# Kernel tuning notes

Hardware: AMD Instinct MI355X
Metric: run time of the kernel (lower is better)

The kernel has to match this reference:

```python
import jax, jax.numpy as jnp
import numpy as np

N_NODES = 100000
N_EDGES = 1600000
HID = 128
EDGE_DIM = 32
GN_EPS = 1e-5


def setup_inputs() -> dict:
    key = jax.random.key(0)
    ks = jax.random.split(key, 8)
    s = 0.05
    return {
        "x": jax.random.normal(ks[0], (N_NODES, HID), jnp.float32),
        "edge_index": jax.random.randint(ks[1], (2, N_EDGES), 0, N_NODES, jnp.int64),
        "edge_attr": jax.random.normal(ks[2], (N_EDGES, EDGE_DIM), jnp.float32),
        "edge_lin_W": jax.random.normal(ks[3], (EDGE_DIM, HID), jnp.float32) * s,
        "edge_lin_b": jnp.zeros((HID,), jnp.float32),
        "mlp_W1": jax.random.normal(ks[4], (HID, HID), jnp.float32) * s,
        "mlp_b1": jnp.zeros((HID,), jnp.float32),
        "mlp_W2": jax.random.normal(ks[5], (HID, HID), jnp.float32) * s,
        "mlp_b2": jnp.zeros((HID,), jnp.float32),
        "gn_weight": jnp.ones((HID,), jnp.float32),
        "gn_bias": jnp.zeros((HID,), jnp.float32),
        "gn_mean_scale": jnp.ones((HID,), jnp.float32),
    }


def reference(x, edge_index, edge_attr, edge_lin_W, edge_lin_b,
              mlp_W1, mlp_b1, mlp_W2, mlp_b2,
              gn_weight, gn_bias, gn_mean_scale):
    src, dst = edge_index[0], edge_index[1]
    # GINEConv message: ReLU(x_j + Lin(edge_attr)), sum-aggregated at dst
    e = edge_attr @ edge_lin_W + edge_lin_b            # [E, HID]
    msg = jax.nn.relu(x[src] + e)                      # [E, HID]
    agg = jax.ops.segment_sum(msg, dst, num_segments=x.shape[0])  # [N, HID]
    # update MLP on (1+eps)*x + agg, eps = 0
    h = agg + x
    h = jax.nn.relu(h @ mlp_W1 + mlp_b1) @ mlp_W2 + mlp_b2
    # GraphNorm with batch=None -> single graph: global node stats
    mean = jnp.mean(h, axis=0, keepdims=True)          # [1, HID]
    sub = h - gn_mean_scale * mean
    var = jnp.mean(sub * sub, axis=0, keepdims=True)
    out = gn_weight * sub / jnp.sqrt(var + GN_EPS) + gn_bias
    # final ReLU; dropout is identity at eval
    return jax.nn.relu(out)
```

## Files before the change

### kernel.cpp

```cpp
#include <hip/hip_runtime.h>
#include <stdint.h>

#define HID 128
#define EDIM 32

typedef __attribute__((ext_vector_type(8))) short bf16x8;
typedef __attribute__((ext_vector_type(4))) float f4_t;

static __device__ __forceinline__ unsigned short f2bf(float f) {
  union { float f; unsigned int u; } v; v.f = f;
  return (unsigned short)((v.u + 0x7fffu + ((v.u >> 16) & 1u)) >> 16);
}

static __device__ __forceinline__ float bf2f(short s) {
  union { unsigned int u; float f; } v;
  v.u = ((unsigned int)(unsigned short)s) << 16;
  return v.f;
}

static __device__ __forceinline__ void atomAddF(float* p, float v) {
#if defined(__gfx950__) || defined(__gfx942__) || defined(__gfx90a__)
  unsafeAtomicAdd(p, v);
#else
  atomicAdd(p, v);
#endif
}

__global__ __launch_bounds__(256) void hist_xperm(const int* __restrict__ ei,
                                                  const float* __restrict__ x,
                                                  unsigned int* __restrict__ counts,
                                                  unsigned short* __restrict__ xPerm,
                                                  int nE, int nNodes, int doPerm) {
  int tid = blockIdx.x * blockDim.x + threadIdx.x;
  const int stride = gridDim.x * blockDim.x;
  for (int i = tid; i < nE; i += stride) atomicAdd(&counts[ei[nE + i]], 1u);
  if (doPerm) {
    const int nCh = nNodes * 16;
    for (int j = tid; j < nCh; j += stride) {
      const int node = j >> 4, g = j & 15;
      const float* xp = x + (size_t)node * HID + g;
      bf16x8 o;
#pragma unroll
      for (int k = 0; k < 8; ++k) o[k] = (short)f2bf(xp[k * 16]);
      *(bf16x8*)(xPerm + (size_t)node * HID + g * 8) = o;
    }
  }
}

__global__ __launch_bounds__(1024) void chunk_sum(const unsigned int* __restrict__ counts,
                                                  unsigned int* __restrict__ chunkSum, int N) {
  __shared__ unsigned int wsum[16];
  const int tid = threadIdx.x;
  const int i = blockIdx.x * 1024 + tid;
  unsigned int v = (i < N) ? counts[i] : 0u;
#pragma unroll
  for (int d = 1; d < 64; d <<= 1) v += (unsigned int)__shfl_xor((int)v, d);
  if ((tid & 63) == 0) wsum[tid >> 6] = v;
  __syncthreads();
  if (tid < 16) {
    unsigned int t = wsum[tid];
#pragma unroll
    for (int d = 1; d < 16; d <<= 1) t += (unsigned int)__shfl_xor((int)t, d);
    if (tid == 0) chunkSum[blockIdx.x] = t;
  }
}

__global__ __launch_bounds__(256) void scan_chunks(const unsigned int* __restrict__ chunkSum,
                                                   unsigned int* __restrict__ chunkOff,
                                                   unsigned int* __restrict__ offsets,
                                                   int nChunks, int N) {
  __shared__ unsigned int wsum[4];
  const int tid = threadIdx.x, lane = tid & 63, w = tid >> 6;
  unsigned int v = (tid < nChunks) ? chunkSum[tid] : 0u;
  unsigned int s = v;
#pragma unroll
  for (int d = 1; d < 64; d <<= 1) {
    unsigned int t = (unsigned int)__shfl_up((int)s, d);
    if (lane >= d) s += t;
  }
  if (lane == 63) wsum[w] = s;
  __syncthreads();
  unsigned int wOff = 0;
  for (int k = 0; k < w; ++k) wOff += wsum[k];
  if (tid < nChunks) chunkOff[tid] = wOff + s - v;
  if (tid == nChunks - 1) offsets[N] = wOff + s;
}

__global__ __launch_bounds__(1024) void scan_local(const unsigned int* __restrict__ counts,
                                                   const unsigned int* __restrict__ chunkOff,
                                                   unsigned int* __restrict__ offsets,
                                                   unsigned int* __restrict__ cursors, int N) {
  __shared__ unsigned int wsum[16];
  const int tid = threadIdx.x, lane = tid & 63, w = tid >> 6;
  const int i = blockIdx.x * 1024 + tid;
  unsigned int v = (i < N) ? counts[i] : 0u;
  unsigned int s = v;
#pragma unroll
  for (int d = 1; d < 64; d <<= 1) {
    unsigned int t = (unsigned int)__shfl_up((int)s, d);
    if (lane >= d) s += t;
  }
  if (lane == 63) wsum[w] = s;
  __syncthreads();
  unsigned int wOff = 0;
  for (int k = 0; k < w; ++k) wOff += wsum[k];
  if (i < N) {
    const unsigned int ex = chunkOff[blockIdx.x] + wOff + (s - v);
    offsets[i] = ex;
    cursors[i] = ex;
  }
}

__global__ __launch_bounds__(256) void scatter_conv(const int* __restrict__ ei,
                                                    const float* __restrict__ ea,
                                                    unsigned int* __restrict__ cursors,
                                                    unsigned int* __restrict__ sortedSrc,
                                                    unsigned short* __restrict__ eaSorted,
                                                    int nE) {
  const int lane = threadIdx.x & 63;
  const int q = lane & 3;
  int t = blockIdx.x * blockDim.x + threadIdx.x;
  const int eStride = (gridDim.x * blockDim.x) >> 2;
  for (int e = t >> 2; e < nE; e += eStride) {
    unsigned int pos = 0;
    if (q == 0) {
      const int d = ei[nE + e];
      pos = atomicAdd(&cursors[d], 1u);
      sortedSrc[pos] = (unsigned int)ei[e];
    }
    pos = (unsigned int)__shfl((int)pos, lane & ~3);
    const f4_t* ap = (const f4_t*)(ea + (size_t)e * EDIM + q * 8);
    f4_t a0 = __builtin_nontemporal_load(ap);
    f4_t a1 = __builtin_nontemporal_load(ap + 1);
    bf16x8 o;
#pragma unroll
    for (int k = 0; k < 4; ++k) { o[k] = (short)f2bf(a0[k]); o[k + 4] = (short)f2bf(a1[k]); }
    *(bf16x8*)(eaSorted + (size_t)pos * EDIM + q * 8) = o;
  }
}

__global__ __launch_bounds__(256) void scatter_min(const int* __restrict__ ei,
                                                   unsigned int* __restrict__ cursors,
                                                   unsigned int* __restrict__ sortedEid,
                                                   unsigned int* __restrict__ sortedSrc,
                                                   int nE) {
  int i = blockIdx.x * blockDim.x + threadIdx.x;
  const int stride = gridDim.x * blockDim.x;
  for (; i < nE; i += stride) {
    const int d = ei[nE + i];
    const unsigned int pos = atomicAdd(&cursors[d], 1u);
    sortedEid[pos] = (unsigned int)i;
    sortedSrc[pos] = (unsigned int)ei[i];
  }
}

template <int MODE>
__global__ __launch_bounds__(256) void agg_kernel(
    const float* __restrict__ x, const unsigned short* __restrict__ xPerm,
    const float* __restrict__ ea, const unsigned short* __restrict__ eaSorted,
    const float* __restrict__ W, const float* __restrict__ bias,
    const unsigned int* __restrict__ offsets, const unsigned int* __restrict__ sortedEid,
    const unsigned int* __restrict__ sortedSrc, float* __restrict__ h,
    int nNodes) {
  const int lane = threadIdx.x & 63;
  const int l15 = lane & 15;
  const int lq  = lane >> 4;

  bf16x8 Wf[8];
  float bv[8];
#pragma unroll
  for (int nt = 0; nt < 8; ++nt) {
#pragma unroll
    for (int j = 0; j < 8; ++j)
      Wf[nt][j] = (short)f2bf(W[(8 * lq + j) * HID + 16 * nt + l15]);
    bv[nt] = bias[16 * nt + l15];
  }

  const int wavesPerBlk = blockDim.x >> 6;
  int waveId = blockIdx.x * wavesPerBlk + ((int)threadIdx.x >> 6);
  const int nWaves = gridDim.x * wavesPerBlk;

  for (int n = waveId; n < nNodes; n += nWaves) {
    const unsigned int beg = offsets[n];
    const unsigned int end = offsets[n + 1];

    float accv[8] = {0, 0, 0, 0, 0, 0, 0, 0};

    for (unsigned int base = beg; base < end; base += 16) {
      bf16x8 af = {0, 0, 0, 0, 0, 0, 0, 0};
      const unsigned int slotA = base + (unsigned int)l15;
      if (slotA < end) {
        if (MODE == 2) {
          const unsigned int eidA = __builtin_nontemporal_load(&sortedEid[slotA]);
          const float* ap = ea + (size_t)eidA * EDIM + 8 * lq;
          f4_t a0 = *(const f4_t*)ap;
          f4_t a1 = *(const f4_t*)(ap + 4);
#pragma unroll
          for (int j = 0; j < 4; ++j) { af[j] = (short)f2bf(a0[j]); af[j + 4] = (short)f2bf(a1[j]); }
        } else {
          af = __builtin_nontemporal_load(
              (const bf16x8*)(eaSorted + (size_t)slotA * EDIM + lq * 8));
        }
      }

      unsigned int s_r[4];
      bf16x8 xg[4];
#pragma unroll
      for (int r = 0; r < 4; ++r) {
        unsigned int slot = base + (unsigned int)(lq * 4 + r);
        unsigned int cl = slot < end ? slot : end - 1;
        s_r[r] = sortedSrc[cl];
        if (MODE == 0)
          xg[r] = *(const bf16x8*)(xPerm + (size_t)s_r[r] * HID + l15 * 8);
      }

      f4_t acc[8];
#pragma unroll
      for (int nt = 0; nt < 8; ++nt) {
        f4_t c; c[0] = bv[nt]; c[1] = bv[nt]; c[2] = bv[nt]; c[3] = bv[nt];
        acc[nt] = __builtin_amdgcn_mfma_f32_16x16x32_bf16(af, Wf[nt], c, 0, 0, 0);
      }

#pragma unroll
      for (int r = 0; r < 4; ++r) {
        const unsigned int slot = base + (unsigned int)(lq * 4 + r);
        if (slot < end) {
          if (MODE == 0) {
#pragma unroll
            for (int nt = 0; nt < 8; ++nt)
              accv[nt] += fmaxf(acc[nt][r] + bf2f(xg[r][nt]), 0.f);
          } else {
            const float* xp = x + (size_t)s_r[r] * HID + l15;
#pragma unroll
            for (int nt = 0; nt < 8; ++nt)
              accv[nt] += fmaxf(acc[nt][r] + xp[nt * 16], 0.f);
          }
        }
      }
    }

#pragma unroll
    for (int nt = 0; nt < 8; ++nt) {
      accv[nt] += __shfl_xor(accv[nt], 16);
      accv[nt] += __shfl_xor(accv[nt], 32);
    }

    const int c0 = 32 * lq + l15;
    const size_t rowOff = (size_t)n * HID;
    h[rowOff + c0]      = accv[2 * lq]     + x[rowOff + c0];
    h[rowOff + c0 + 16] = accv[2 * lq + 1] + x[rowOff + c0 + 16];
  }
}

__global__ __launch_bounds__(256) void node_kernel(
    float* __restrict__ h, const float* __restrict__ W1, const float* __restrict__ b1,
    const float* __restrict__ W2, const float* __restrict__ b2,
    float* __restrict__ stats, int nNodes, int nTiles) {
  __shared__ unsigned short sW1[128 * 128];
  __shared__ unsigned short sW2[128 * 128];
  __shared__ unsigned short sH1[4][16 * 128];

  for (int idx = threadIdx.x; idx < 128 * 128; idx += 256) {
    int n = idx & 127, k = idx >> 7;
    int off = n * 128 + ((((k >> 3) ^ (n & 15))) << 3) + (k & 7);
    sW1[off] = f2bf(W1[k * HID + n]);
    sW2[off] = f2bf(W2[k * HID + n]);
  }
  __syncthreads();

  const int lane = threadIdx.x & 63;
  const int l15 = lane & 15, lq = lane >> 4;
  const int wv = threadIdx.x >> 6;
  unsigned short* hb = &sH1[wv][0];

  float b1v[8], b2v[8];
#pragma unroll
  for (int nt = 0; nt < 8; ++nt) { b1v[nt] = b1[nt * 16 + l15]; b2v[nt] = b2[nt * 16 + l15]; }
  float ssum[8] = {0, 0, 0, 0, 0, 0, 0, 0};
  float ssq[8]  = {0, 0, 0, 0, 0, 0, 0, 0};

  int waveId = blockIdx.x * 4 + wv;
  const int nWaves = gridDim.x * 4;

  for (int tile = waveId; tile < nTiles; tile += nWaves) {
    const int r0 = tile << 4;
    int rr = r0 + l15; if (rr >= nNodes) rr = nNodes - 1;
    const float* hp = h + (size_t)rr * HID;

    bf16x8 af[4];
#pragma unroll
    for (int kt = 0; kt < 4; ++kt) {
      const int k0 = kt * 32 + 8 * lq;
      f4_t u0 = *(const f4_t*)(hp + k0);
      f4_t u1 = *(const f4_t*)(hp + k0 + 4);
#pragma unroll
      for (int j = 0; j < 4; ++j) {
        af[kt][j]     = (short)f2bf(u0[j]);
        af[kt][j + 4] = (short)f2bf(u1[j]);
      }
    }

    f4_t acc[8];
#pragma unroll
    for (int nt = 0; nt < 8; ++nt) {
      f4_t c; c[0] = b1v[nt]; c[1] = b1v[nt]; c[2] = b1v[nt]; c[3] = b1v[nt];
#pragma unroll
      for (int kt = 0; kt < 4; ++kt) {
        bf16x8 wf = *(const bf16x8*)&sW1[(nt * 16 + l15) * 128 + ((((kt * 4 + lq) ^ l15)) << 3)];
        c = __builtin_amdgcn_mfma_f32_16x16x32_bf16(af[kt], wf, c, 0, 0, 0);
      }
      acc[nt] = c;
    }

#pragma unroll
    for (int nt = 0; nt < 8; ++nt) {
      const int ghi = 2 * nt + (l15 >> 3);
#pragma unroll
      for (int r = 0; r < 4; ++r) {
        const int row = lq * 4 + r;
        hb[row * 128 + ((ghi ^ (row & 15)) << 3) + (l15 & 7)] = f2bf(fmaxf(acc[nt][r], 0.f));
      }
    }
    asm volatile("s_waitcnt lgkmcnt(0)" ::: "memory");
    __builtin_amdgcn_sched_barrier(0);

    bf16x8 af2[4];
#pragma unroll
    for (int kt = 0; kt < 4; ++kt)
      af2[kt] = *(const bf16x8*)&hb[l15 * 128 + ((((kt * 4 + lq) ^ l15)) << 3)];

    f4_t acc2[8];
#pragma unroll
    for (int nt = 0; nt < 8; ++nt) {
      f4_t c; c[0] = b2v[nt]; c[1] = b2v[nt]; c[2] = b2v[nt]; c[3] = b2v[nt];
#pragma unroll
      for (int kt = 0; kt < 4; ++kt) {
        bf16x8 wf = *(const bf16x8*)&sW2[(nt * 16 + l15) * 128 + ((((kt * 4 + lq) ^ l15)) << 3)];
        c = __builtin_amdgcn_mfma_f32_16x16x32_bf16(af2[kt], wf, c, 0, 0, 0);
      }
      acc2[nt] = c;
    }

#pragma unroll
    for (int nt = 0; nt < 8; ++nt) {
#pragma unroll
      for (int r = 0; r < 4; ++r) {
        const int row = r0 + lq * 4 + r;
        if (row < nNodes) {
          float v = acc2[nt][r];
          h[(size_t)row * HID + nt * 16 + l15] = v;
          ssum[nt] += v; ssq[nt] += v * v;
        }
      }
    }
  }

#pragma unroll
  for (int nt = 0; nt < 8; ++nt) {
    float a = ssum[nt], b = ssq[nt];
    a += __shfl_xor(a, 16); b += __shfl_xor(b, 16);
    a += __shfl_xor(a, 32); b += __shfl_xor(b, 32);
    if (lq == 0) {
      atomAddF(&stats[nt * 16 + l15], a);
      atomAddF(&stats[HID + nt * 16 + l15], b);
    }
  }
}

__global__ void norm_prep(float* __restrict__ stats, const float* __restrict__ gw,
                          const float* __restrict__ gb, const float* __restrict__ gs,
                          int nNodes) {
  int c = threadIdx.x;
  if (c < HID) {
    float invN = 1.f / (float)nNodes;
    float m   = stats[c] * invN;
    float msq = stats[HID + c] * invN;
    float s   = gs[c];
    float var = msq - (2.f * s - s * s) * m * m;
    float A = gw[c] * rsqrtf(var + 1e-5f);
    float B = gb[c] - A * s * m;
    stats[2 * HID + c] = A;
    stats[3 * HID + c] = B;
  }
}

__global__ __launch_bounds__(256) void norm_kernel(const float* __restrict__ stats,
                                                   float* __restrict__ out, int total4) {
  const f4_t* A4 = (const f4_t*)(stats + 2 * HID);
  const f4_t* B4 = (const f4_t*)(stats + 3 * HID);
  int i = blockIdx.x * blockDim.x + threadIdx.x;
  const int stride = gridDim.x * blockDim.x;
  for (; i < total4; i += stride) {
    const int cg = i & 31;
    f4_t h = ((const f4_t*)out)[i];
    f4_t a = A4[cg], b = B4[cg];
    f4_t o;
#pragma unroll
    for (int j = 0; j < 4; ++j) o[j] = fmaxf(fmaf(h[j], a[j], b[j]), 0.f);
    ((f4_t*)out)[i] = o;
  }
}

extern "C" void kernel_launch(void* const* d_in, const int* in_sizes, int n_in,
                              void* d_out, int out_size, void* d_ws, size_t ws_size,
                              hipStream_t stream) {
  const float* x  = (const float*)d_in[0];
  const int*   ei = (const int*)d_in[1];
  const float* ea = (const float*)d_in[2];
  const float* eW = (const float*)d_in[3];
  const float* eb = (const float*)d_in[4];
  const float* W1 = (const float*)d_in[5];
  const float* b1 = (const float*)d_in[6];
  const float* W2 = (const float*)d_in[7];
  const float* b2 = (const float*)d_in[8];
  const float* gw = (const float*)d_in[9];
  const float* gb = (const float*)d_in[10];
  const float* gs = (const float*)d_in[11];
  float* out = (float*)d_out;

  const int nNodes = in_sizes[0] / HID;
  const int nE     = in_sizes[1] / 2;

  char* w = (char*)d_ws;
  const size_t offStats   = 0;
  const size_t offCounts  = 2048;
  const size_t offCursors = offCounts  + (size_t)nNodes * 4;
  const size_t offOffsets = offCursors + (size_t)nNodes * 4;
  const size_t offChunk   = offOffsets + (size_t)(nNodes + 16) * 4;
  const size_t offSSrc    = offChunk   + 2048;
  const size_t base0      = offSSrc    + (size_t)nE * 4;
  const size_t needB = base0 + (size_t)nE * EDIM * 2;
  const size_t needA = needB + (size_t)nNodes * HID * 2;

  float* stats            = (float*)(w + offStats);
  unsigned int* counts    = (unsigned int*)(w + offCounts);
  unsigned int* cursors   = (unsigned int*)(w + offCursors);
  unsigned int* offsets   = (unsigned int*)(w + offOffsets);
  unsigned int* chunkSum  = (unsigned int*)(w + offChunk);
  unsigned int* chunkOff  = (unsigned int*)(w + offChunk + 1024);
  unsigned int* sortedSrc = (unsigned int*)(w + offSSrc);
  unsigned int* sortedEid = (unsigned int*)(w + base0);
  unsigned short* eaSorted= (unsigned short*)(w + base0);
  unsigned short* xPerm   = (unsigned short*)(w + needB);

  const int mode = (ws_size >= needA) ? 0 : (ws_size >= needB ? 1 : 2);

  hipMemsetAsync(d_ws, 0, offCursors, stream);

  hist_xperm<<<2048, 256, 0, stream>>>(ei, x, counts, xPerm, nE, nNodes, mode == 0 ? 1 : 0);

  const int nChunks = (nNodes + 1023) / 1024;
  chunk_sum<<<nChunks, 1024, 0, stream>>>(counts, chunkSum, nNodes);
  scan_chunks<<<1, 256, 0, stream>>>(chunkSum, chunkOff, offsets, nChunks, nNodes);
  scan_local<<<nChunks, 1024, 0, stream>>>(counts, chunkOff, offsets, cursors, nNodes);

  if (mode == 2)
    scatter_min<<<1024, 256, 0, stream>>>(ei, cursors, sortedEid, sortedSrc, nE);
  else
    scatter_conv<<<2048, 256, 0, stream>>>(ei, ea, cursors, sortedSrc, eaSorted, nE);

  if (mode == 0)
    agg_kernel<0><<<8192, 256, 0, stream>>>(x, xPerm, ea, eaSorted, eW, eb, offsets, sortedEid, sortedSrc, out, nNodes);
  else if (mode == 1)
    agg_kernel<1><<<8192, 256, 0, stream>>>(x, xPerm, ea, eaSorted, eW, eb, offsets, sortedEid, sortedSrc, out, nNodes);
  else
    agg_kernel<2><<<8192, 256, 0, stream>>>(x, xPerm, ea, eaSorted, eW, eb, offsets, sortedEid, sortedSrc, out, nNodes);

  const int nTiles = (nNodes + 15) >> 4;
  node_kernel<<<782, 256, 0, stream>>>(out, W1, b1, W2, b2, stats, nNodes, nTiles);

  norm_prep<<<1, 128, 0, stream>>>(stats, gw, gb, gs, nNodes);
  norm_kernel<<<2048, 256, 0, stream>>>(stats, out, nNodes * (HID / 4));
}
```

Before: 472.2 us.

## Aggregate edges over 16-node ranges with LDS atomics and prefetch

Replaces the one-wave-per-node aggregation with one wave per range of 16 consecutive destination nodes. The wave processes that range's sorted edges as a flat stream of 16-edge MFMA tiles, so tiles are no longer padded per node, and it accumulates messages into LDS with atomics keyed by destination. The scatter now stores (src,dst) pairs so each tile knows its destinations, and the next tile's loads are software-prefetched. This removes per-node tile underutilisation at about 16 edges per node, at the cost of LDS atomic contention, 32 KB of LDS per block, and a changed node_kernel grid size.

```diff
diff --git a/kernel.cpp b/kernel.cpp
--- a/kernel.cpp
+++ b/kernel.cpp
@@ -3,6 +3,7 @@
 
 #define HID 128
 #define EDIM 32
+#define NPW 16
 
 typedef __attribute__((ext_vector_type(8))) short bf16x8;
 typedef __attribute__((ext_vector_type(4))) float f4_t;
@@ -114,7 +115,7 @@
 __global__ __launch_bounds__(256) void scatter_conv(const int* __restrict__ ei,
                                                     const float* __restrict__ ea,
                                                     unsigned int* __restrict__ cursors,
-                                                    unsigned int* __restrict__ sortedSrc,
+                                                    uint2* __restrict__ sortedSD,
                                                     unsigned short* __restrict__ eaSorted,
                                                     int nE) {
   const int lane = threadIdx.x & 63;
@@ -126,7 +127,7 @@
     if (q == 0) {
       const int d = ei[nE + e];
       pos = atomicAdd(&cursors[d], 1u);
-      sortedSrc[pos] = (unsigned int)ei[e];
+      sortedSD[pos] = make_uint2((unsigned int)ei[e], (unsigned int)d);
     }
     pos = (unsigned int)__shfl((int)pos, lane & ~3);
     const f4_t* ap = (const f4_t*)(ea + (size_t)e * EDIM + q * 8);
@@ -154,17 +155,18 @@
   }
 }
 
-template <int MODE>
-__global__ __launch_bounds__(256) void agg_kernel(
+__global__ __launch_bounds__(256) void agg_flat(
     const float* __restrict__ x, const unsigned short* __restrict__ xPerm,
-    const float* __restrict__ ea, const unsigned short* __restrict__ eaSorted,
+    const unsigned short* __restrict__ eaSorted, const uint2* __restrict__ sortedSD,
     const float* __restrict__ W, const float* __restrict__ bias,
-    const unsigned int* __restrict__ offsets, const unsigned int* __restrict__ sortedEid,
-    const unsigned int* __restrict__ sortedSrc, float* __restrict__ h,
-    int nNodes) {
+    const unsigned int* __restrict__ offsets, float* __restrict__ h,
+    int nNodes, int nRanges) {
+  __shared__ float accL[4][NPW][HID];
   const int lane = threadIdx.x & 63;
   const int l15 = lane & 15;
   const int lq  = lane >> 4;
+  const int wv  = threadIdx.x >> 6;
+  float* al = &accL[wv][0][0];
 
   bf16x8 Wf[8];
   float bv[8];
@@ -176,65 +178,140 @@
     bv[nt] = bias[16 * nt + l15];
   }
 
-  const int wavesPerBlk = blockDim.x >> 6;
-  int waveId = blockIdx.x * wavesPerBlk + ((int)threadIdx.x >> 6);
-  const int nWaves = gridDim.x * wavesPerBlk;
+  int waveId = blockIdx.x * 4 + wv;
+  const int nWaves = gridDim.x * 4;
+
+  for (int rng = waveId; rng < nRanges; rng += nWaves) {
+    const int n0 = rng * NPW;
+    const int n1 = min(n0 + NPW, nNodes);
+    const unsigned int begR = offsets[n0];
+    const unsigned int endR = offsets[n1];
+
+    for (int i = lane; i < NPW * HID; i += 64) al[i] = 0.f;
+
+    if (begR < endR) {
+      auto LOADT = [&](unsigned int b, bf16x8& af, bf16x8* xg, int& dpack) {
+        const unsigned int sA = b + (unsigned int)l15;
+        if (sA < endR)
+          af = __builtin_nontemporal_load(
+              (const bf16x8*)(eaSorted + (size_t)sA * EDIM + lq * 8));
+        else
+          af = bf16x8{0, 0, 0, 0, 0, 0, 0, 0};
+        dpack = 0;
+#pragma unroll
+        for (int r = 0; r < 4; ++r) {
+          unsigned int sl = b + (unsigned int)(lq * 4 + r);
+          unsigned int cl = sl < endR ? sl : endR - 1;
+          uint2 sd = sortedSD[cl];
+          dpack |= (int)((sd.y - (unsigned int)n0) & 15u) << (4 * r);
+          xg[r] = *(const bf16x8*)(xPerm + (size_t)sd.x * HID + l15 * 8);
+        }
+      };
+
+      bf16x8 afA, xgA[4];
+      int dpA;
+      unsigned int base = begR;
+      LOADT(base, afA, xgA, dpA);
+
+      while (true) {
+        const unsigned int nb = base + 16;
+        const bool more = nb < endR;
+        bf16x8 afB, xgB[4];
+        int dpB = 0;
+        if (more) LOADT(nb, afB, xgB, dpB);
+
+        f4_t acc[8];
+#pragma unroll
+        for (int nt = 0; nt < 8; ++nt) {
+          f4_t c; c[0] = bv[nt]; c[1] = bv[nt]; c[2] = bv[nt]; c[3] = bv[nt];
+          acc[nt] = __builtin_amdgcn_mfma_f32_16x16x32_bf16(afA, Wf[nt], c, 0, 0, 0);
+        }
+
+#pragma unroll
+        for (int r = 0; r < 4; ++r) {
+          const unsigned int slot = base + (unsigned int)(lq * 4 + r);
+          if (slot < endR) {
+            const int d = (dpA >> (4 * r)) & 15;
+            float* ap = al + d * HID + l15;
+#pragma unroll
+            for (int k = 0; k < 8; ++k) {
+              const int nt = (k + lq) & 7;
+              atomicAdd(ap + nt * 16, fmaxf(acc[nt][r] + bf2f(xgA[r][nt]), 0.f));
+            }
+          }
+        }
+
+        if (!more) break;
+        afA = afB;
+#pragma unroll
+        for (int r = 0; r < 4; ++r) xgA[r] = xgB[r];
+        dpA = dpB;
+        base = nb;
+      }
+    }
+
+    asm volatile("s_waitcnt lgkmcnt(0)" ::: "memory");
+    const int nOut = (n1 - n0) * HID;
+    for (int i = lane; i < nOut; i += 64) {
+      const size_t g = (size_t)n0 * HID + i;
+      h[g] = al[i] + x[g];
+    }
+  }
+}
+
+__global__ __launch_bounds__(256) void agg_fb(
+    const float* __restrict__ x, const float* __restrict__ ea,
+    const float* __restrict__ W, const float* __restrict__ bias,
+    const unsigned int* __restrict__ offsets, const unsigned int* __restrict__ sortedEid,
+    const unsigned int* __restrict__ sortedSrc, float* __restrict__ h, int nNodes) {
+  const int lane = threadIdx.x & 63;
+  const int l15 = lane & 15;
+  const int lq  = lane >> 4;
+
+  bf16x8 Wf[8];
+  float bv[8];
+#pragma unroll
+  for (int nt = 0; nt < 8; ++nt) {
+#pragma unroll
+    for (int j = 0; j < 8; ++j)
+      Wf[nt][j] = (short)f2bf(W[(8 * lq + j) * HID + 16 * nt + l15]);
+    bv[nt] = bias[16 * nt + l15];
+  }
+
+  int waveId = blockIdx.x * 4 + ((int)threadIdx.x >> 6);
+  const int nWaves = gridDim.x * 4;
 
   for (int n = waveId; n < nNodes; n += nWaves) {
     const unsigned int beg = offsets[n];
     const unsigned int end = offsets[n + 1];
-
     float accv[8] = {0, 0, 0, 0, 0, 0, 0, 0};
 
     for (unsigned int base = beg; base < end; base += 16) {
       bf16x8 af = {0, 0, 0, 0, 0, 0, 0, 0};
       const unsigned int slotA = base + (unsigned int)l15;
       if (slotA < end) {
-        if (MODE == 2) {
-          const unsigned int eidA = __builtin_nontemporal_load(&sortedEid[slotA]);
-          const float* ap = ea + (size_t)eidA * EDIM + 8 * lq;
-          f4_t a0 = *(const f4_t*)ap;
-          f4_t a1 = *(const f4_t*)(ap + 4);
-#pragma unroll
-          for (int j = 0; j < 4; ++j) { af[j] = (short)f2bf(a0[j]); af[j + 4] = (short)f2bf(a1[j]); }
-        } else {
-          af = __builtin_nontemporal_load(
-              (const bf16x8*)(eaSorted + (size_t)slotA * EDIM + lq * 8));
-        }
-      }
-
-      unsigned int s_r[4];
-      bf16x8 xg[4];
-#pragma unroll
-      for (int r = 0; r < 4; ++r) {
-        unsigned int slot = base + (unsigned int)(lq * 4 + r);
-        unsigned int cl = slot < end ? slot : end - 1;
-        s_r[r] = sortedSrc[cl];
-        if (MODE == 0)
-          xg[r] = *(const bf16x8*)(xPerm + (size_t)s_r[r] * HID + l15 * 8);
-      }
-
+        const unsigned int eidA = sortedEid[slotA];
+        const float* ap = ea + (size_t)eidA * EDIM + 8 * lq;
+        f4_t a0 = *(const f4_t*)ap;
+        f4_t a1 = *(const f4_t*)(ap + 4);
+#pragma unroll
+        for (int j = 0; j < 4; ++j) { af[j] = (short)f2bf(a0[j]); af[j + 4] = (short)f2bf(a1[j]); }
+      }
       f4_t acc[8];
 #pragma unroll
       for (int nt = 0; nt < 8; ++nt) {
         f4_t c; c[0] = bv[nt]; c[1] = bv[nt]; c[2] = bv[nt]; c[3] = bv[nt];
         acc[nt] = __builtin_amdgcn_mfma_f32_16x16x32_bf16(af, Wf[nt], c, 0, 0, 0);
       }
-
 #pragma unroll
       for (int r = 0; r < 4; ++r) {
         const unsigned int slot = base + (unsigned int)(lq * 4 + r);
         if (slot < end) {
-          if (MODE == 0) {
-#pragma unroll
-            for (int nt = 0; nt < 8; ++nt)
-              accv[nt] += fmaxf(acc[nt][r] + bf2f(xg[r][nt]), 0.f);
-          } else {
-            const float* xp = x + (size_t)s_r[r] * HID + l15;
-#pragma unroll
-            for (int nt = 0; nt < 8; ++nt)
-              accv[nt] += fmaxf(acc[nt][r] + xp[nt * 16], 0.f);
-          }
+          const int s = (int)sortedSrc[slot];
+          const float* xp = x + (size_t)s * HID + l15;
+#pragma unroll
+          for (int nt = 0; nt < 8; ++nt)
+            accv[nt] += fmaxf(acc[nt][r] + xp[nt * 16], 0.f);
         }
       }
     }
@@ -244,7 +321,6 @@
       accv[nt] += __shfl_xor(accv[nt], 16);
       accv[nt] += __shfl_xor(accv[nt], 32);
     }
-
     const int c0 = 32 * lq + l15;
     const size_t rowOff = (size_t)n * HID;
     h[rowOff + c0]      = accv[2 * lq]     + x[rowOff + c0];
@@ -426,11 +502,12 @@
   const size_t offCounts  = 2048;
   const size_t offCursors = offCounts  + (size_t)nNodes * 4;
   const size_t offOffsets = offCursors + (size_t)nNodes * 4;
-  const size_t offChunk   = offOffsets + (size_t)(nNodes + 16) * 4;
-  const size_t offSSrc    = offChunk   + 2048;
-  const size_t base0      = offSSrc    + (size_t)nE * 4;
-  const size_t needB = base0 + (size_t)nE * EDIM * 2;
-  const size_t needA = needB + (size_t)nNodes * HID * 2;
+  const size_t offChunk   = offOffsets + (((size_t)(nNodes + 1) * 4 + 63) & ~63ull);
+  const size_t offSD      = (offChunk + 2048 + 7) & ~7ull;
+  const size_t offEaS     = offSD + (size_t)nE * 8;
+  const size_t offXP      = offEaS + (size_t)nE * EDIM * 2;
+  const size_t needFlat   = offXP + (size_t)nNodes * HID * 2;
+  const size_t needFb     = offSD + (size_t)nE * 8;
 
   float* stats            = (float*)(w + offStats);
   unsigned int* counts    = (unsigned int*)(w + offCounts);
@@ -438,36 +515,37 @@
   unsigned int* offsets   = (unsigned int*)(w + offOffsets);
   unsigned int* chunkSum  = (unsigned int*)(w + offChunk);
   unsigned int* chunkOff  = (unsigned int*)(w + offChunk + 1024);
-  unsigned int* sortedSrc = (unsigned int*)(w + offSSrc);
-  unsigned int* sortedEid = (unsigned int*)(w + base0);
-  unsigned short* eaSorted= (unsigned short*)(w + base0);
-  unsigned short* xPerm   = (unsigned short*)(w + needB);
-
-  const int mode = (ws_size >= needA) ? 0 : (ws_size >= needB ? 1 : 2);
+  uint2*        sortedSD  = (uint2*)(w + offSD);
+  unsigned int* sortedEid = (unsigned int*)(w + offSD);
+  unsigned int* sortedSrc = (unsigned int*)(w + offSD + (size_t)nE * 4);
+  unsigned short* eaSorted= (unsigned short*)(w + offEaS);
+  unsigned short* xPerm   = (unsigned short*)(w + offXP);
+
+  const int flatMode = (ws_size >= needFlat) ? 1 : 0;
+  (void)needFb;
 
   hipMemsetAsync(d_ws, 0, offCursors, stream);
 
-  hist_xperm<<<2048, 256, 0, stream>>>(ei, x, counts, xPerm, nE, nNodes, mode == 0 ? 1 : 0);
+  hist_xperm<<<2048, 256, 0, stream>>>(ei, x, counts, xPerm, nE, nNodes, flatMode);
 
   const int nChunks = (nNodes + 1023) / 1024;
   chunk_sum<<<nChunks, 1024, 0, stream>>>(counts, chunkSum, nNodes);
   scan_chunks<<<1, 256, 0, stream>>>(chunkSum, chunkOff, offsets, nChunks, nNodes);
   scan_local<<<nChunks, 1024, 0, stream>>>(counts, chunkOff, offsets, cursors, nNodes);
 
-  if (mode == 2)
+  if (flatMode) {
+    scatter_conv<<<2048, 256, 0, stream>>>(ei, ea, cursors, sortedSD, eaSorted, nE);
+    const int nRanges = (nNodes + NPW - 1) / NPW;
+    const int blocks = (nRanges + 3) / 4;
+    agg_flat<<<blocks, 256, 0, stream>>>(x, xPerm, eaSorted, sortedSD, eW, eb,
+                                         offsets, out, nNodes, nRanges);
+  } else {
     scatter_min<<<1024, 256, 0, stream>>>(ei, cursors, sortedEid, sortedSrc, nE);
-  else
-    scatter_conv<<<2048, 256, 0, stream>>>(ei, ea, cursors, sortedSrc, eaSorted, nE);
-
-  if (mode == 0)
-    agg_kernel<0><<<8192, 256, 0, stream>>>(x, xPerm, ea, eaSorted, eW, eb, offsets, sortedEid, sortedSrc, out, nNodes);
-  else if (mode == 1)
-    agg_kernel<1><<<8192, 256, 0, stream>>>(x, xPerm, ea, eaSorted, eW, eb, offsets, sortedEid, sortedSrc, out, nNodes);
-  else
-    agg_kernel<2><<<8192, 256, 0, stream>>>(x, xPerm, ea, eaSorted, eW, eb, offsets, sortedEid, sortedSrc, out, nNodes);
+    agg_fb<<<8192, 256, 0, stream>>>(x, ea, eW, eb, offsets, sortedEid, sortedSrc, out, nNodes);
+  }
 
   const int nTiles = (nNodes + 15) >> 4;
-  node_kernel<<<782, 256, 0, stream>>>(out, W1, b1, W2, b2, stats, nNodes, nTiles);
+  node_kernel<<<512, 256, 0, stream>>>(out, W1, b1, W2, b2, stats, nNodes, nTiles);
 
   norm_prep<<<1, 128, 0, stream>>>(stats, gw, gb, gs, nNodes);
   norm_kernel<<<2048, 256, 0, stream>>>(stats, out, nNodes * (HID / 4));
```

Measured after the change: 1.473 ms. +212.0%, slower.
